# Kernel tuning notes

Measured on AMD Instinct MI355X. Metric: run time of the kernel, lower is better.

## Reference

```python
import jax, jax.numpy as jnp
import numpy as np
import math

EPS = 1e-08
S = 64.0
MARGIN = 0.5
COS_M = math.cos(MARGIN)
SIN_M = math.sin(MARGIN)
B, D, C = 1024, 256, 200000


def setup_inputs() -> dict:
    key = jax.random.key(0)
    k1, k2, k3 = jax.random.split(key, 3)
    embeddings = jax.random.normal(k1, (B, D), dtype=jnp.float32)
    labels = jax.random.randint(k2, (B,), 0, C, dtype=jnp.int64)
    # xavier_uniform for prototypes [C, D]
    limit = math.sqrt(6.0 / (C + D))
    prototypes = jax.random.uniform(k3, (C, D), dtype=jnp.float32, minval=-limit, maxval=limit)
    return {"embeddings": embeddings, "labels": labels, "prototypes": prototypes}


def _l2norm(x):
    # torch F.normalize: x / max(||x||, 1e-12)
    n = jnp.sqrt(jnp.sum(x * x, axis=-1, keepdims=True))
    return x / jnp.maximum(n, 1e-12)


def reference(embeddings, labels, prototypes):
    e = _l2norm(embeddings)            # [B, D]
    p = _l2norm(prototypes)            # [C, D]
    cos_theta = jnp.einsum('bd,cd->bc', e, p)  # [B, C]
    sine_theta = jnp.clip(jnp.sqrt(jnp.maximum(1.0 - cos_theta * cos_theta, EPS)), EPS, 1.0 - EPS)
    phi = cos_theta * COS_M - sine_theta * SIN_M
    # apply margin only on the true-class column, then scale
    mask = jax.nn.one_hot(labels, C, dtype=cos_theta.dtype)
    logits = S * (mask * phi + (1.0 - mask) * cos_theta)
    logp = jax.nn.log_softmax(logits, axis=-1)
    loss = -jnp.mean(jnp.take_along_axis(logp, labels[:, None], axis=1))
    return loss
```

## Files before the change

kernel.cpp:

```cpp
#include <hip/hip_runtime.h>
#include <cstdint>
#include <cstddef>

#define D_DIM   256
#define B_ROWS  1024
#define C_CLS   200000
#define S_SC    64.0f
#define S_LOG2E 92.33248261689366f
#define COS_M_F 0.87758256189037271612f
#define SIN_M_F 0.47942553860420300027f
#define EPS_F   1e-8f

#define CT 256
#define BT 128
#define NCT 782
#define CPAD (NCT * CT)
#define NPADROW (CPAD - C_CLS)
#define NBLK (NCT * 8)

typedef int   i32x4  __attribute__((ext_vector_type(4)));
typedef int   i32x8  __attribute__((ext_vector_type(8)));
typedef float f32x16 __attribute__((ext_vector_type(16)));

__device__ __forceinline__ float fast_exp_s(float x) {
  return __builtin_amdgcn_exp2f(S_LOG2E * x);
}

__global__ void k_norm_all8(const float* __restrict__ emb,
                            const float* __restrict__ proto,
                            unsigned char* __restrict__ ebf8,
                            unsigned char* __restrict__ pbf8,
                            float* __restrict__ sums,
                            float* __restrict__ out) {
  int wid = threadIdx.x >> 6, lane = threadIdx.x & 63;
  int idx = (blockIdx.x << 2) + wid;
  const float* src;
  unsigned char* dst;
  if (idx < CPAD) {
    if (idx >= C_CLS) {
      *reinterpret_cast<unsigned int*>(pbf8 + (size_t)idx * D_DIM + lane * 4) = 0u;
      return;
    }
    src = proto + (size_t)idx * D_DIM;
    dst = pbf8 + (size_t)idx * D_DIM;
  } else {
    int row = idx - CPAD;
    if (lane == 0) sums[row] = 0.0f;
    if (idx == CPAD && lane == 1) *out = 0.0f;
    src = emb + (size_t)row * D_DIM;
    dst = ebf8 + (size_t)row * D_DIM;
  }
  const float4 v = *reinterpret_cast<const float4*>(src + lane * 4);
  float ss = v.x * v.x + v.y * v.y + v.z * v.z + v.w * v.w;
#pragma unroll
  for (int m = 32; m >= 1; m >>= 1) ss += __shfl_xor(ss, m, 64);
  float inv = 1.0f / fmaxf(sqrtf(ss), 1e-12f);
  int packed = 0;
  packed = __builtin_amdgcn_cvt_pk_fp8_f32(v.x * inv, v.y * inv, packed, false);
  packed = __builtin_amdgcn_cvt_pk_fp8_f32(v.z * inv, v.w * inv, packed, true);
  *reinterpret_cast<int*>(dst + lane * 4) = packed;
}

__global__ __launch_bounds__(512, 4) void k_gemm_sw(
    const unsigned char* __restrict__ ebf8, const unsigned char* __restrict__ pbf8,
    float* __restrict__ sums) {
  __shared__ __align__(16) unsigned char Pls[CT * 256];
  __shared__ float bsum[BT];

  const int t = threadIdx.x;
  const int lane = t & 63;
  const int rsel = lane & 31;
  const int h = lane >> 5;
  const int wv = t >> 6;
  const int wc = wv >> 2;
  const int wb = wv & 3;

  int bid = (int)blockIdx.x;
  int w = (bid & 7) * NCT + (bid >> 3);
  const int ct = w >> 3;
  const int bt = w & 7;
  const int c0 = ct * CT;
  const int b0 = bt * BT;

#pragma unroll
  for (int j = 0; j < 8; ++j) {
    int G = j * 512 + t;
    int r = G >> 4, p = G & 15;
    int lg = p ^ (r & 15);
    const unsigned char* g = pbf8 + (size_t)(c0 + r) * D_DIM + lg * 16;
    __builtin_amdgcn_global_load_lds(
        (const __attribute__((address_space(1))) unsigned int*)(const void*)g,
        (__attribute__((address_space(3))) unsigned int*)(void*)(Pls + G * 16),
        16, 0, 0);
  }
  if (t < BT) bsum[t] = 0.0f;

  f32x16 acc[4];
#pragma unroll
  for (int mi = 0; mi < 4; ++mi)
#pragma unroll
    for (int e = 0; e < 16; ++e) acc[mi][e] = 0.0f;

  asm volatile("s_waitcnt vmcnt(0)" ::: "memory");
  __syncthreads();

  const unsigned char* ebase =
      ebf8 + (size_t)(b0 + wb * 32 + rsel) * D_DIM + h * 32;
#pragma unroll
  for (int ks = 0; ks < 4; ++ks) {
    i32x4 blo = *reinterpret_cast<const i32x4*>(ebase + ks * 64);
    i32x4 bhi = *reinterpret_cast<const i32x4*>(ebase + ks * 64 + 16);
    i32x8 bf = __builtin_shufflevector(blo, bhi, 0, 1, 2, 3, 4, 5, 6, 7);
    const int g = ks * 4 + h * 2;
#pragma unroll
    for (int mi = 0; mi < 4; ++mi) {
      int r = wc * 128 + mi * 32 + rsel;
      int p0 = g ^ (r & 15), p1 = (g + 1) ^ (r & 15);
      i32x4 lo = *reinterpret_cast<const i32x4*>(Pls + r * 256 + p0 * 16);
      i32x4 hi = *reinterpret_cast<const i32x4*>(Pls + r * 256 + p1 * 16);
      i32x8 af = __builtin_shufflevector(lo, hi, 0, 1, 2, 3, 4, 5, 6, 7);
      acc[mi] = __builtin_amdgcn_mfma_scale_f32_32x32x64_f8f6f4(
          af, bf, acc[mi], 0, 0,
          0, 0x7F7F7F7F, 0, 0x7F7F7F7F);
    }
  }

  float bp = 0.0f;
#pragma unroll
  for (int mi = 0; mi < 4; ++mi)
#pragma unroll
    for (int reg = 0; reg < 16; ++reg)
      bp += fast_exp_s(acc[mi][reg]);
  bp += __shfl_xor(bp, 32, 64);
  if (lane < 32) atomicAdd(&bsum[wb * 32 + rsel], bp);
  __syncthreads();
  if (t < BT) atomicAdd(&sums[b0 + t], bsum[t]);
}

__device__ __forceinline__ float f8tof(unsigned char u) {
  int e = (u >> 3) & 15, m = u & 7;
  float mag = e ? ldexpf((float)(8 + m), e - 10) : ldexpf((float)m, -9);
  return (u & 0x80) ? -mag : mag;
}

__global__ void k_finalize(const unsigned char* __restrict__ ebf8,
                           const unsigned char* __restrict__ pbf8,
                           const int* __restrict__ labels,
                           const float* __restrict__ sums,
                           float* __restrict__ out) {
  __shared__ float part[4];
  int wid = threadIdx.x >> 6, lane = threadIdx.x & 63;
  int b = (blockIdx.x << 2) + wid;
  int lab = labels[b];
  const unsigned char* e = ebf8 + (size_t)b * D_DIM + lane * 4;
  const unsigned char* p = pbf8 + (size_t)lab * D_DIM + lane * 4;
  unsigned int eu = *reinterpret_cast<const unsigned int*>(e);
  unsigned int pu = *reinterpret_cast<const unsigned int*>(p);
  float dot = 0.0f;
#pragma unroll
  for (int i = 0; i < 4; ++i)
    dot += f8tof((eu >> (8 * i)) & 0xff) * f8tof((pu >> (8 * i)) & 0xff);
#pragma unroll
  for (int m = 32; m >= 1; m >>= 1) dot += __shfl_xor(dot, m, 64);
  if (lane == 0) {
    float cs = dot;
    float sn = sqrtf(fmaxf(1.0f - cs * cs, EPS_F));
    sn = fminf(fmaxf(sn, EPS_F), 1.0f - EPS_F);
    float phi = cs * COS_M_F - sn * SIN_M_F;
    float sp = S_SC * phi;
    float total = sums[b] - (float)NPADROW - fast_exp_s(cs) + __expf(sp);
    part[wid] = logf(total) - sp;
  }
  __syncthreads();
  if (threadIdx.x == 0) {
    float s = part[0] + part[1] + part[2] + part[3];
    atomicAdd(out, s * (1.0f / (float)B_ROWS));
  }
}

extern "C" void kernel_launch(void* const* d_in, const int* in_sizes, int n_in,
                              void* d_out, int out_size, void* d_ws, size_t ws_size,
                              hipStream_t stream) {
  const float* emb    = (const float*)d_in[0];
  const int*   labels = (const int*)d_in[1];
  const float* proto  = (const float*)d_in[2];
  float* out = (float*)d_out;

  char* ws = (char*)d_ws;
  unsigned char* ebf8 = (unsigned char*)ws;
  float* sums = (float*)(ws + 262144);
  unsigned char* pbf8 = (unsigned char*)(ws + 2097152);

  k_norm_all8<<<(CPAD + B_ROWS) / 4, 256, 0, stream>>>(emb, proto, ebf8, pbf8,
                                                       sums, out);
  k_gemm_sw<<<NBLK, 512, 0, stream>>>(ebf8, pbf8, sums);
  k_finalize<<<B_ROWS / 4, 256, 0, stream>>>(ebf8, pbf8, labels, sums, out);
}
```

Before: 117.1 us.

## Double batch tile per block and fold exp scaling into MFMA scale factors

Each GEMM block now covers 256 batch rows by looping twice over the same LDS prototype tile, which halves the number of blocks and the prototype LDS loads per batch row. The log2(e) factor is folded into the fp8 prototype normalization and the scale of 64 into the MFMA A-scale exponent (0x85), so the exp loop becomes a bare exp2 with no per-element multiply. The finalize kernel rescales the dot product back by ln2. Folding log2(e) into the stored fp8 values changes their rounding, and the unroll-1 loop serializes the two passes over the tile.

```diff
diff --git a/kernel.cpp b/kernel.cpp
--- a/kernel.cpp
+++ b/kernel.cpp
@@ -6,25 +6,25 @@
 #define B_ROWS  1024
 #define C_CLS   200000
 #define S_SC    64.0f
-#define S_LOG2E 92.33248261689366f
+#define LOG2E_F 1.44269504088896340736f
+#define LN2_F   0.69314718055994530942f
 #define COS_M_F 0.87758256189037271612f
 #define SIN_M_F 0.47942553860420300027f
 #define EPS_F   1e-8f
 
 #define CT 256
-#define BT 128
+#define BT 256
 #define NCT 782
 #define CPAD (NCT * CT)
 #define NPADROW (CPAD - C_CLS)
-#define NBLK (NCT * 8)
+#define NBLK (NCT * 4)
+
+#define SCALE_A 0x85858585
+#define SCALE_1 0x7F7F7F7F
 
 typedef int   i32x4  __attribute__((ext_vector_type(4)));
 typedef int   i32x8  __attribute__((ext_vector_type(8)));
 typedef float f32x16 __attribute__((ext_vector_type(16)));
-
-__device__ __forceinline__ float fast_exp_s(float x) {
-  return __builtin_amdgcn_exp2f(S_LOG2E * x);
-}
 
 __global__ void k_norm_all8(const float* __restrict__ emb,
                             const float* __restrict__ proto,
@@ -36,6 +36,7 @@
   int idx = (blockIdx.x << 2) + wid;
   const float* src;
   unsigned char* dst;
+  float post = 1.0f;
   if (idx < CPAD) {
     if (idx >= C_CLS) {
       *reinterpret_cast<unsigned int*>(pbf8 + (size_t)idx * D_DIM + lane * 4) = 0u;
@@ -43,6 +44,7 @@
     }
     src = proto + (size_t)idx * D_DIM;
     dst = pbf8 + (size_t)idx * D_DIM;
+    post = LOG2E_F;
   } else {
     int row = idx - CPAD;
     if (lane == 0) sums[row] = 0.0f;
@@ -54,7 +56,7 @@
   float ss = v.x * v.x + v.y * v.y + v.z * v.z + v.w * v.w;
 #pragma unroll
   for (int m = 32; m >= 1; m >>= 1) ss += __shfl_xor(ss, m, 64);
-  float inv = 1.0f / fmaxf(sqrtf(ss), 1e-12f);
+  float inv = post / fmaxf(sqrtf(ss), 1e-12f);
   int packed = 0;
   packed = __builtin_amdgcn_cvt_pk_fp8_f32(v.x * inv, v.y * inv, packed, false);
   packed = __builtin_amdgcn_cvt_pk_fp8_f32(v.z * inv, v.w * inv, packed, true);
@@ -76,9 +78,9 @@
   const int wb = wv & 3;
 
   int bid = (int)blockIdx.x;
-  int w = (bid & 7) * NCT + (bid >> 3);
-  const int ct = w >> 3;
-  const int bt = w & 7;
+  int w = (bid & 7) * (NBLK / 8) + (bid >> 3);
+  const int ct = w >> 2;
+  const int bt = w & 3;
   const int c0 = ct * CT;
   const int b0 = bt * BT;
 
@@ -94,45 +96,48 @@
         16, 0, 0);
   }
   if (t < BT) bsum[t] = 0.0f;
-
-  f32x16 acc[4];
-#pragma unroll
-  for (int mi = 0; mi < 4; ++mi)
-#pragma unroll
-    for (int e = 0; e < 16; ++e) acc[mi][e] = 0.0f;
-
   asm volatile("s_waitcnt vmcnt(0)" ::: "memory");
   __syncthreads();
 
-  const unsigned char* ebase =
-      ebf8 + (size_t)(b0 + wb * 32 + rsel) * D_DIM + h * 32;
-#pragma unroll
-  for (int ks = 0; ks < 4; ++ks) {
-    i32x4 blo = *reinterpret_cast<const i32x4*>(ebase + ks * 64);
-    i32x4 bhi = *reinterpret_cast<const i32x4*>(ebase + ks * 64 + 16);
-    i32x8 bf = __builtin_shufflevector(blo, bhi, 0, 1, 2, 3, 4, 5, 6, 7);
-    const int g = ks * 4 + h * 2;
-#pragma unroll
-    for (int mi = 0; mi < 4; ++mi) {
-      int r = wc * 128 + mi * 32 + rsel;
-      int p0 = g ^ (r & 15), p1 = (g + 1) ^ (r & 15);
-      i32x4 lo = *reinterpret_cast<const i32x4*>(Pls + r * 256 + p0 * 16);
-      i32x4 hi = *reinterpret_cast<const i32x4*>(Pls + r * 256 + p1 * 16);
-      i32x8 af = __builtin_shufflevector(lo, hi, 0, 1, 2, 3, 4, 5, 6, 7);
-      acc[mi] = __builtin_amdgcn_mfma_scale_f32_32x32x64_f8f6f4(
-          af, bf, acc[mi], 0, 0,
-          0, 0x7F7F7F7F, 0, 0x7F7F7F7F);
+#pragma unroll 1
+  for (int it = 0; it < 2; ++it) {
+    f32x16 acc[4];
+#pragma unroll
+    for (int mi = 0; mi < 4; ++mi)
+#pragma unroll
+      for (int e = 0; e < 16; ++e) acc[mi][e] = 0.0f;
+
+    const unsigned char* ebase =
+        ebf8 + (size_t)(b0 + it * 128 + wb * 32 + rsel) * D_DIM + h * 32;
+#pragma unroll
+    for (int ks = 0; ks < 4; ++ks) {
+      i32x4 blo = *reinterpret_cast<const i32x4*>(ebase + ks * 64);
+      i32x4 bhi = *reinterpret_cast<const i32x4*>(ebase + ks * 64 + 16);
+      i32x8 bf = __builtin_shufflevector(blo, bhi, 0, 1, 2, 3, 4, 5, 6, 7);
+      const int g = ks * 4 + h * 2;
+#pragma unroll
+      for (int mi = 0; mi < 4; ++mi) {
+        int r = wc * 128 + mi * 32 + rsel;
+        int p0 = g ^ (r & 15), p1 = (g + 1) ^ (r & 15);
+        i32x4 lo = *reinterpret_cast<const i32x4*>(Pls + r * 256 + p0 * 16);
+        i32x4 hi = *reinterpret_cast<const i32x4*>(Pls + r * 256 + p1 * 16);
+        i32x8 af = __builtin_shufflevector(lo, hi, 0, 1, 2, 3, 4, 5, 6, 7);
+        acc[mi] = __builtin_amdgcn_mfma_scale_f32_32x32x64_f8f6f4(
+            af, bf, acc[mi], 0, 0,
+            0, SCALE_A, 0, SCALE_1);
+      }
     }
-  }
-
-  float bp = 0.0f;
-#pragma unroll
-  for (int mi = 0; mi < 4; ++mi)
-#pragma unroll
-    for (int reg = 0; reg < 16; ++reg)
-      bp += fast_exp_s(acc[mi][reg]);
-  bp += __shfl_xor(bp, 32, 64);
-  if (lane < 32) atomicAdd(&bsum[wb * 32 + rsel], bp);
+
+    float bp = 0.0f;
+#pragma unroll
+    for (int mi = 0; mi < 4; ++mi)
+#pragma unroll
+      for (int reg = 0; reg < 16; ++reg)
+        bp += __builtin_amdgcn_exp2f(acc[mi][reg]);
+    bp += __shfl_xor(bp, 32, 64);
+    if (lane < 32) atomicAdd(&bsum[it * 128 + wb * 32 + rsel], bp);
+  }
+
   __syncthreads();
   if (t < BT) atomicAdd(&sums[b0 + t], bsum[t]);
 }
@@ -156,19 +161,20 @@
   const unsigned char* p = pbf8 + (size_t)lab * D_DIM + lane * 4;
   unsigned int eu = *reinterpret_cast<const unsigned int*>(e);
   unsigned int pu = *reinterpret_cast<const unsigned int*>(p);
-  float dot = 0.0f;
+  float dot_s = 0.0f;
 #pragma unroll
   for (int i = 0; i < 4; ++i)
-    dot += f8tof((eu >> (8 * i)) & 0xff) * f8tof((pu >> (8 * i)) & 0xff);
-#pragma unroll
-  for (int m = 32; m >= 1; m >>= 1) dot += __shfl_xor(dot, m, 64);
+    dot_s += f8tof((eu >> (8 * i)) & 0xff) * f8tof((pu >> (8 * i)) & 0xff);
+#pragma unroll
+  for (int m = 32; m >= 1; m >>= 1) dot_s += __shfl_xor(dot_s, m, 64);
   if (lane == 0) {
-    float cs = dot;
+    float cs = dot_s * LN2_F;
     float sn = sqrtf(fmaxf(1.0f - cs * cs, EPS_F));
     sn = fminf(fmaxf(sn, EPS_F), 1.0f - EPS_F);
     float phi = cs * COS_M_F - sn * SIN_M_F;
     float sp = S_SC * phi;
-    float total = sums[b] - (float)NPADROW - fast_exp_s(cs) + __expf(sp);
+    float el = __builtin_amdgcn_exp2f(S_SC * dot_s);
+    float total = sums[b] - (float)NPADROW - el + __expf(sp);
     part[wid] = logf(total) - sp;
   }
   __syncthreads();
```

New measurement: 341.1 us. 2.91x slower.
